# Optimization experiments

Hardware: AMD Instinct MI355X
Metric: run time of the kernel (lower is better)

## Reference

```python
import jax, jax.numpy as jnp
import numpy as np

B, H, W, C = 16, 64, 64, 256
WS = 8          # window_size
SHIFT = 4       # shift_size
HEADS = 8
HEAD_DIM = C // HEADS
N = WS * WS     # tokens per window
HID = 4 * C     # mlp hidden
EPS = 1e-5


def _rel_pos_index():
    coords = np.stack(np.meshgrid(np.arange(WS), np.arange(WS), indexing='ij'))  # [2,WS,WS]
    flat = coords.reshape(2, -1)                                                  # [2,N]
    rel = (flat[:, :, None] - flat[:, None, :]).transpose(1, 2, 0)                # [N,N,2]
    rel[:, :, 0] += WS - 1
    rel[:, :, 1] += WS - 1
    rel[:, :, 0] *= 2 * WS - 1
    return rel.sum(-1).astype(np.int32)                                           # [N,N]


def _attn_mask():
    # shifted-window region ids, identical to get_img_mask (shift == WS//2)
    img = np.zeros((H, W), dtype=np.float32)
    cnt = 0
    for hs in (slice(0, H - WS), slice(H - WS, H - SHIFT), slice(H - SHIFT, H)):
        for ws_ in (slice(0, W - WS), slice(W - WS, W - SHIFT), slice(W - SHIFT, W)):
            img[hs, ws_] = cnt
            cnt += 1
    mw = img.reshape(H // WS, WS, W // WS, WS).transpose(0, 2, 1, 3).reshape(-1, N)  # [nW,N]
    diff = mw[:, None, :] - mw[:, :, None]
    return np.where(diff != 0, -100.0, 0.0).astype(np.float32)                        # [nW,N,N]


def window_partition(x):
    # [B,H,W,C] -> [B*nW, N, C]
    x = x.reshape(B, H // WS, WS, W // WS, WS, C)
    return x.transpose(0, 1, 3, 2, 4, 5).reshape(-1, N, C)


def window_reverse(w):
    # [B*nW, WS, WS, C] -> [B,H,W,C]
    x = w.reshape(B, H // WS, W // WS, WS, WS, C)
    return x.transpose(0, 1, 3, 2, 4, 5).reshape(B, H, W, C)


def layernorm(x, g, b):
    mu = jnp.mean(x, -1, keepdims=True)
    var = jnp.mean(jnp.square(x - mu), -1, keepdims=True)
    return (x - mu) * jax.lax.rsqrt(var + EPS) * g + b


def setup_inputs() -> dict:
    key = jax.random.key(0)
    ks = jax.random.split(key, 12)
    s = 0.02
    return {
        'x': jax.random.normal(ks[0], (B, H, W, C), jnp.float32),
        'ln1_g': jnp.ones((C,), jnp.float32),
        'ln1_b': jnp.zeros((C,), jnp.float32),
        'qkv_w': jax.random.normal(ks[1], (C, 3 * C), jnp.float32) * s,
        'qkv_b': jnp.zeros((3 * C,), jnp.float32),
        'proj_w': jax.random.normal(ks[2], (C, C), jnp.float32) * s,
        'proj_b': jnp.zeros((C,), jnp.float32),
        'rel_bias_table': jax.random.normal(ks[3], ((2 * WS - 1) ** 2, HEADS), jnp.float32) * s,
        'ln2_g': jnp.ones((C,), jnp.float32),
        'ln2_b': jnp.zeros((C,), jnp.float32),
        'mlp_w1': jax.random.normal(ks[4], (C, HID), jnp.float32) * s,
        'mlp_b1': jnp.zeros((HID,), jnp.float32),
        'mlp_w2': jax.random.normal(ks[5], (HID, C), jnp.float32) * s,
        'mlp_b2': jnp.zeros((C,), jnp.float32),
        'rel_index': jnp.asarray(_rel_pos_index()),  # [N,N] int32, constant
    }


def reference(x, ln1_g, ln1_b, qkv_w, qkv_b, proj_w, proj_b, rel_bias_table,
              ln2_g, ln2_b, mlp_w1, mlp_b1, mlp_w2, mlp_b2, rel_index):
    attn_mask = jnp.asarray(_attn_mask())                 # [nW,N,N]
    nW = attn_mask.shape[0]

    shortcut = x.reshape(B, H * W, C)
    h = layernorm(shortcut, ln1_g, ln1_b).reshape(B, H, W, C)

    # cyclic shift + window partition
    h = jnp.roll(h, shift=(-SHIFT, -SHIFT), axis=(1, 2))
    xw = window_partition(h)                              # [B*nW, N, C]

    # window attention with relative position bias
    qkv = xw @ qkv_w + qkv_b                              # [B*nW, N, 3C]
    qkv = qkv.reshape(-1, N, 3, HEADS, HEAD_DIM).transpose(2, 0, 3, 1, 4)
    q, k, v = qkv[0], qkv[1], qkv[2]                      # [B*nW, heads, N, hd]
    attn = jnp.einsum('whnd,whmd->whnm', q * (HEAD_DIM ** -0.5), k)
    bias = rel_bias_table[rel_index]                      # [N,N,heads]
    attn = attn + bias.transpose(2, 0, 1)[None]           # [B*nW,heads,N,N]
    attn = attn.reshape(B, nW, HEADS, N, N) + attn_mask[None, :, None]
    attn = jax.nn.softmax(attn.reshape(-1, HEADS, N, N), axis=-1)
    out = jnp.einsum('whnm,whmd->whnd', attn, v)
    out = out.transpose(0, 2, 1, 3).reshape(-1, N, C)
    out = out @ proj_w + proj_b                           # [B*nW, N, C]

    # window reverse + reverse shift
    out = window_reverse(out.reshape(-1, WS, WS, C))
    out = jnp.roll(out, shift=(SHIFT, SHIFT), axis=(1, 2)).reshape(B, H * W, C)

    h = shortcut + out
    m = layernorm(h, ln2_g, ln2_b)
    m = jax.nn.gelu(m @ mlp_w1 + mlp_b1) @ mlp_w2 + mlp_b2
    h = h + m
    return h.reshape(B, H, W, C)
```

## Files before the change

kernel.cpp:

```cpp
#include <hip/hip_runtime.h>


typedef __attribute__((ext_vector_type(8))) short bf16x8;
typedef __attribute__((ext_vector_type(4))) float f32x4;
typedef __attribute__((ext_vector_type(16))) float f32x16;

__device__ __forceinline__ float bf2f(unsigned short h) {
    union { unsigned int u; float f; } c; c.u = ((unsigned int)h) << 16; return c.f;
}
__device__ __forceinline__ unsigned short f2bf(float f) {
    union { float f; unsigned int u; } c; c.f = f;
    unsigned int u = c.u;
    return (unsigned short)((u + 0x7FFFu + ((u >> 16) & 1u)) >> 16);
}
__device__ __forceinline__ unsigned int cvtpk_bf16(float lo, float hi) {
    unsigned int r;
    asm volatile("v_cvt_pk_bf16_f32 %0, %1, %2" : "=v"(r) : "v"(lo), "v"(hi));
    return r;
}
__device__ __forceinline__ void perm32swap(unsigned int& a, unsigned int& b) {
    asm volatile("v_permlane32_swap_b32 %0, %1" : "+v"(a), "+v"(b));
}
__device__ __forceinline__ int remap_row(int row) {
    int b  = row >> 12;
    int w6 = (row >> 6) & 63;
    int n  = row & 63;
    int hp = (((w6 >> 3) << 3) + (n >> 3) + 4) & 63;
    int wp = (((w6 & 7) << 3) + (n & 7) + 4) & 63;
    return (b << 12) | (hp << 6) | wp;
}
__device__ __forceinline__ float gelu_f(float v) {
    float u = 1.5957691216057308f * (v + 0.044715f * v * v * v);
    return v / (1.0f + __expf(-u));
}
__device__ __forceinline__ void gload16(const unsigned short* g, unsigned short* l) {
    __builtin_amdgcn_global_load_lds(
        (const __attribute__((address_space(1))) void*)g,
        (__attribute__((address_space(3))) void*)l, 16, 0, 0);
}

template<int INBF>
__global__ __launch_bounds__(256) void ln_kernel(
    const void* __restrict__ inp, const float* __restrict__ g,
    const float* __restrict__ b, unsigned short* __restrict__ out, int remap)
{
    int wave = threadIdx.x >> 6, lane = threadIdx.x & 63;
    int row = (blockIdx.x << 2) + wave;
    int src = remap ? remap_row(row) : row;
    float4 xv;
    if (INBF) {
        ushort4 u = *(const ushort4*)((const unsigned short*)inp + (size_t)src * 256 + (lane << 2));
        xv.x = bf2f(u.x); xv.y = bf2f(u.y); xv.z = bf2f(u.z); xv.w = bf2f(u.w);
    } else {
        xv = *(const float4*)((const float*)inp + (size_t)src * 256 + (lane << 2));
    }
    float s  = xv.x + xv.y + xv.z + xv.w;
    float ss = xv.x*xv.x + xv.y*xv.y + xv.z*xv.z + xv.w*xv.w;
#pragma unroll
    for (int off = 32; off; off >>= 1) {
        s  += __shfl_xor(s,  off, 64);
        ss += __shfl_xor(ss, off, 64);
    }
    float mu  = s * (1.0f / 256.0f);
    float inv = rsqrtf(ss * (1.0f / 256.0f) - mu * mu + 1e-5f);
    float4 gv = *(const float4*)(g + (lane << 2));
    float4 bv = *(const float4*)(b + (lane << 2));
    ushort4 o;
    o.x = f2bf((xv.x - mu) * inv * gv.x + bv.x);
    o.y = f2bf((xv.y - mu) * inv * gv.y + bv.y);
    o.z = f2bf((xv.z - mu) * inv * gv.z + bv.z);
    o.w = f2bf((xv.w - mu) * inv * gv.w + bv.w);
    *(ushort4*)(out + (size_t)row * 256 + (lane << 2)) = o;
}

__device__ __forceinline__ void convT_body(
    const float* __restrict__ in, unsigned short* __restrict__ out,
    int K, int N, int b, float (*t)[33], int tid)
{
    int kb = K >> 5;
    int bk = (b % kb) << 5;
    int bn = (b / kb) << 5;
    int r = tid >> 5, c = tid & 31;
#pragma unroll
    for (int i = 0; i < 4; ++i)
        t[r + i * 8][c] = in[(size_t)(bk + r + i * 8) * N + bn + c];
    __syncthreads();
#pragma unroll
    for (int i = 0; i < 4; ++i)
        out[(size_t)(bn + r + i * 8) * K + bk + c] = f2bf(t[c][r + i * 8]);
}

__global__ __launch_bounds__(256) void prep_kernel(
    const float* __restrict__ qkv_w, const float* __restrict__ proj_w,
    const float* __restrict__ w1, const float* __restrict__ w2,
    unsigned short* __restrict__ qkvT, unsigned short* __restrict__ prjT,
    unsigned short* __restrict__ w1T, unsigned short* __restrict__ w2T,
    const float* __restrict__ table, const int* __restrict__ relidx,
    float* __restrict__ bexp)
{
    __shared__ float t[32][33];
    const int b = blockIdx.x, tid = threadIdx.x;
    if      (b < 192) convT_body(qkv_w, qkvT, 256,  768, b,       t, tid);
    else if (b < 256) convT_body(proj_w, prjT, 256,  256, b - 192, t, tid);
    else if (b < 512) convT_body(w1,    w1T,  256, 1024, b - 256, t, tid);
    else if (b < 768) convT_body(w2,    w2T, 1024,  256, b - 512, t, tid);
    else {
        int i = (b - 768) * 256 + tid;
        int head = i >> 12;
        int q = (i >> 6) & 63;
        int k = i & 63;
        bexp[i] = table[relidx[q * 64 + k] * 8 + head];
    }
}

template<int OUT_BF16, int DO_GELU, int RESID, int QSCALE, int RESBF>
__global__ __launch_bounds__(512, 2) void mgemm_kernel(
    const unsigned short* __restrict__ A, const unsigned short* __restrict__ BT,
    const float* __restrict__ bias, void* __restrict__ outp,
    const void* __restrict__ resid, int M, int N, int K)
{
    __shared__ __align__(16) unsigned short smem[32768];
#define ASB(b) (smem + (b) * 4096)
#define BSB(b) (smem + 16384 + (b) * 4096)

    const int cpx = (int)gridDim.x >> 3;
    const int bid = ((int)blockIdx.x & 7) * cpx + ((int)blockIdx.x >> 3);

    const int nb = N >> 7;
    const int m0 = (bid / nb) << 7;
    const int n0 = (bid % nb) << 7;
    const int tid  = threadIdx.x;
    const int wid  = tid >> 6;
    const int lane = tid & 63;
    const int wm = (wid >> 1) << 5;
    const int wn = (wid & 1) << 6;

    const unsigned short* Ag = A  + (size_t)m0 * K;
    const unsigned short* Bg = BT + (size_t)n0 * K;
    const size_t ra = (size_t)(tid >> 2) * K + (((tid & 3) ^ ((tid >> 2) & 3)) << 3);

    f32x4 acc[4][2] = {};
    const int fr = lane & 15;
    const int fq = lane >> 4;
    const int axor = ((fq ^ (fr & 3)) << 3);

#define STAGE(buf, kk)                                                        \
    {                                                                         \
        gload16(Ag + ra + (kk), ASB(buf) + tid * 8);                          \
        gload16(Bg + ra + (kk), BSB(buf) + tid * 8);                          \
    }

    const int NIT = K >> 5;
    STAGE(0, 0);
    STAGE(1, 32);
    STAGE(2, 64);

    for (int t = 0; t < NIT; ++t) {
        if (t + 2 < NIT)      asm volatile("s_waitcnt vmcnt(4)" ::: "memory");
        else if (t + 1 < NIT) asm volatile("s_waitcnt vmcnt(2)" ::: "memory");
        else                  asm volatile("s_waitcnt vmcnt(0)" ::: "memory");
        __builtin_amdgcn_s_barrier();

        const int cur = t & 3;
        bf16x8 af[2], bfr[4];
#pragma unroll
        for (int i = 0; i < 2; ++i)
            af[i] = *(const bf16x8*)(ASB(cur) + (wm + i * 16 + fr) * 32 + axor);
#pragma unroll
        for (int j = 0; j < 4; ++j)
            bfr[j] = *(const bf16x8*)(BSB(cur) + (wn + j * 16 + fr) * 32 + axor);
#pragma unroll
        for (int j = 0; j < 4; ++j)
#pragma unroll
            for (int i = 0; i < 2; ++i)
                acc[j][i] = __builtin_amdgcn_mfma_f32_16x16x32_bf16(
                    bfr[j], af[i], acc[j][i], 0, 0, 0);

        if (t + 3 < NIT) STAGE((t + 3) & 3, (t + 3) << 5);
    }
#undef STAGE

    __builtin_amdgcn_s_barrier();

#pragma unroll
    for (int j = 0; j < 4; ++j) {
        const int fc = wn + j * 16 + (fq << 2);
        const int gcol = n0 + fc;
        const float4 b4 = *(const float4*)(bias + gcol);
#pragma unroll
        for (int i = 0; i < 2; ++i) {
            const int row = wm + i * 16 + fr;
            float v0 = acc[j][i][0] + b4.x;
            float v1 = acc[j][i][1] + b4.y;
            float v2 = acc[j][i][2] + b4.z;
            float v3 = acc[j][i][3] + b4.w;
            if (QSCALE && gcol < 256) {
                v0 *= 0.17677669529663687f; v1 *= 0.17677669529663687f;
                v2 *= 0.17677669529663687f; v3 *= 0.17677669529663687f;
            }
            if (DO_GELU) {
                v0 = gelu_f(v0); v1 = gelu_f(v1); v2 = gelu_f(v2); v3 = gelu_f(v3);
            }
            if (OUT_BF16) {
                uint2 pp;
                pp.x = cvtpk_bf16(v0, v1);
                pp.y = cvtpk_bf16(v2, v3);
                const int u = (row << 5) + ((fc >> 2) ^ (row & 6));
                *(uint2*)((char*)smem + (size_t)u * 8) = pp;
            } else {
                float4 o4; o4.x = v0; o4.y = v1; o4.z = v2; o4.w = v3;
                const int u = (row << 5) + ((fc >> 2) ^ (row & 7));
                *(float4*)((char*)smem + (size_t)u * 16) = o4;
            }
        }
    }
    __builtin_amdgcn_s_barrier();

    if (OUT_BF16) {
#pragma unroll
        for (int p = 0; p < 4; ++p) {
            const int row = (p << 5) + (tid >> 4);
            const int q = tid & 15;
            const int u = (row << 5) + ((q << 1) ^ (row & 6));
            uint4 a = *(const uint4*)((const char*)smem + (size_t)u * 8);
            const int grow = m0 + row;
            const int orow = (RESID == 2) ? remap_row(grow) : grow;
            const int gcol = n0 + (q << 3);
            if (RESID) {
                float rv[8];
                if (RESBF) {
                    ushort4 ra_ = *(const ushort4*)((const unsigned short*)resid
                                                    + (size_t)orow * N + gcol);
                    ushort4 rb_ = *(const ushort4*)((const unsigned short*)resid
                                                    + (size_t)orow * N + gcol + 4);
                    rv[0]=bf2f(ra_.x); rv[1]=bf2f(ra_.y); rv[2]=bf2f(ra_.z); rv[3]=bf2f(ra_.w);
                    rv[4]=bf2f(rb_.x); rv[5]=bf2f(rb_.y); rv[6]=bf2f(rb_.z); rv[7]=bf2f(rb_.w);
                } else {
                    float4 ra_ = *(const float4*)((const float*)resid + (size_t)orow * N + gcol);
                    float4 rb_ = *(const float4*)((const float*)resid + (size_t)orow * N + gcol + 4);
                    rv[0]=ra_.x; rv[1]=ra_.y; rv[2]=ra_.z; rv[3]=ra_.w;
                    rv[4]=rb_.x; rv[5]=rb_.y; rv[6]=rb_.z; rv[7]=rb_.w;
                }
                const unsigned short* s = (const unsigned short*)&a;
                uint4 o;
                o.x = cvtpk_bf16(bf2f(s[0]) + rv[0], bf2f(s[1]) + rv[1]);
                o.y = cvtpk_bf16(bf2f(s[2]) + rv[2], bf2f(s[3]) + rv[3]);
                o.z = cvtpk_bf16(bf2f(s[4]) + rv[4], bf2f(s[5]) + rv[5]);
                o.w = cvtpk_bf16(bf2f(s[6]) + rv[6], bf2f(s[7]) + rv[7]);
                a = o;
            }
            *(uint4*)((unsigned short*)outp + (size_t)orow * N + gcol) = a;
        }
    } else {
#pragma unroll
        for (int p = 0; p < 8; ++p) {
            const int row = (p << 4) + (tid >> 5);
            const int q = tid & 31;
            const int u = (row << 5) + (q ^ (row & 7));
            float4 v = *(const float4*)((const char*)smem + (size_t)u * 16);
            const int grow = m0 + row;
            const int orow = (RESID == 2) ? remap_row(grow) : grow;
            const int gcol = n0 + (q << 2);
            if (RESID) {
                if (RESBF) {
                    ushort4 r4 = *(const ushort4*)((const unsigned short*)resid
                                                   + (size_t)orow * N + gcol);
                    v.x += bf2f(r4.x); v.y += bf2f(r4.y);
                    v.z += bf2f(r4.z); v.w += bf2f(r4.w);
                } else {
                    float4 r4 = *(const float4*)((const float*)resid + (size_t)orow * N + gcol);
                    v.x += r4.x; v.y += r4.y; v.z += r4.z; v.w += r4.w;
                }
            }
            *(float4*)((float*)outp + (size_t)orow * N + gcol) = v;
        }
    }
#undef ASB
#undef BSB
}

__global__ __launch_bounds__(512, 1) void qkvattn_kernel(
    const unsigned short* __restrict__ xw,
    const unsigned short* __restrict__ qkvT,
    const float* __restrict__ qkv_b,
    const float* __restrict__ bexp,
    unsigned short* __restrict__ out)
{
    __shared__ __align__(16) unsigned short Asm[16384];
    const int widx = blockIdx.x;
    const int tid  = threadIdx.x;
    const int head = tid >> 6;
    const int l    = tid & 63;
    const int lo   = l & 31, hi = l >> 5;

    {
        const unsigned short* Ag = xw + ((size_t)widx << 6) * 256;
#pragma unroll
        for (int i = 0; i < 4; ++i) {
            int u = tid + (i << 9);
            int r = u >> 5, p = u & 31;
            int lg = (p & 24) | ((p ^ r) & 7);
            gload16(Ag + (size_t)r * 256 + lg * 8, Asm + u * 8);
        }
        asm volatile("s_waitcnt vmcnt(0)" ::: "memory");
        __builtin_amdgcn_s_barrier();
    }

#define AREAD(tok, kk)                                                         \
    (*(const bf16x8*)(Asm + (tok) * 256 +                                      \
        (((((kk) >> 3) + hi) & 24) | (((((kk) >> 3) + hi) ^ (tok)) & 7)) * 8))

#define DANCE(aa, op0, op1)                                                    \
    {                                                                          \
        _Pragma("unroll")                                                      \
        for (int kd_ = 0; kd_ < 2; ++kd_) {                                    \
            const int s8_ = kd_ * 8;                                           \
            unsigned int a0 = cvtpk_bf16((aa)[s8_ + 0], (aa)[s8_ + 1]);        \
            unsigned int b0 = cvtpk_bf16((aa)[s8_ + 4], (aa)[s8_ + 5]);        \
            unsigned int a1 = cvtpk_bf16((aa)[s8_ + 2], (aa)[s8_ + 3]);        \
            unsigned int b1 = cvtpk_bf16((aa)[s8_ + 6], (aa)[s8_ + 7]);        \
            perm32swap(a0, b0);                                                \
            perm32swap(a1, b1);                                                \
            union { unsigned int u[4]; bf16x8 v; } w_;                         \
            w_.u[0] = a0; w_.u[1] = a1; w_.u[2] = b0; w_.u[3] = b1;            \
            if (kd_) (op1) = w_.v; else (op0) = w_.v;                          \
        }                                                                      \
    }

    bf16x8 opK[2][2], opQ[2][2];

#pragma unroll
    for (int mat = 0; mat < 2; ++mat) {
        const int sec = mat ? 0 : 1;
        const unsigned short* Wb = qkvT + ((size_t)(sec * 256 + head * 32 + lo)) * 256 + 8 * hi;
        bf16x8 wf[16];
#pragma unroll
        for (int kk = 0; kk < 16; ++kk)
            wf[kk] = *(const bf16x8*)(Wb + kk * 16);
        f32x16 ac[2] = {};
#pragma unroll
        for (int kk = 0; kk < 16; ++kk) {
            ac[0] = __builtin_amdgcn_mfma_f32_32x32x16_bf16(
                wf[kk], AREAD(lo,      kk * 16), ac[0], 0, 0, 0);
            ac[1] = __builtin_amdgcn_mfma_f32_32x32x16_bf16(
                wf[kk], AREAD(lo + 32, kk * 16), ac[1], 0, 0, 0);
        }
        const float* bb = qkv_b + sec * 256 + head * 32 + 4 * hi;
#pragma unroll
        for (int tb = 0; tb < 2; ++tb) {
#pragma unroll
            for (int qd = 0; qd < 4; ++qd) {
                float4 b4 = *(const float4*)(bb + 8 * qd);
                ac[tb][4 * qd + 0] += b4.x;
                ac[tb][4 * qd + 1] += b4.y;
                ac[tb][4 * qd + 2] += b4.z;
                ac[tb][4 * qd + 3] += b4.w;
                if (sec == 0) {
                    ac[tb][4 * qd + 0] *= 0.17677669529663687f;
                    ac[tb][4 * qd + 1] *= 0.17677669529663687f;
                    ac[tb][4 * qd + 2] *= 0.17677669529663687f;
                    ac[tb][4 * qd + 3] *= 0.17677669529663687f;
                }
            }
            if (sec == 1) { DANCE(ac[tb], opK[tb][0], opK[tb][1]); }
            else          { DANCE(ac[tb], opQ[tb][0], opQ[tb][1]); }
        }
    }

    f32x16 acc[2][2] = {};
#pragma unroll
    for (int kd = 0; kd < 2; ++kd) {
        acc[0][0] = __builtin_amdgcn_mfma_f32_32x32x16_bf16(opK[0][kd], opQ[0][kd], acc[0][0], 0, 0, 0);
        acc[0][1] = __builtin_amdgcn_mfma_f32_32x32x16_bf16(opK[0][kd], opQ[1][kd], acc[0][1], 0, 0, 0);
        acc[1][0] = __builtin_amdgcn_mfma_f32_32x32x16_bf16(opK[1][kd], opQ[0][kd], acc[1][0], 0, 0, 0);
        acc[1][1] = __builtin_amdgcn_mfma_f32_32x32x16_bf16(opK[1][kd], opQ[1][kd], acc[1][1], 0, 0, 0);
    }

#pragma unroll
    for (int qb = 0; qb < 2; ++qb) {
        const float* bq = bexp + head * 4096 + (qb * 32 + lo) * 64;
#pragma unroll
        for (int kb = 0; kb < 2; ++kb)
#pragma unroll
            for (int j = 0; j < 4; ++j) {
                float4 b4 = *(const float4*)(bq + kb * 32 + j * 8 + hi * 4);
                acc[kb][qb][4 * j + 0] += b4.x;
                acc[kb][qb][4 * j + 1] += b4.y;
                acc[kb][qb][4 * j + 2] += b4.z;
                acc[kb][qb][4 * j + 3] += b4.w;
            }
    }

    const int w6 = widx & 63;
    if (((w6 >> 3) == 7) || ((w6 & 7) == 7)) {
#pragma unroll
        for (int qb = 0; qb < 2; ++qb) {
            int nq = qb * 32 + lo;
            int phq = ((w6 >> 3) << 3) + (nq >> 3), pwq = ((w6 & 7) << 3) + (nq & 7);
            int rq = ((phq < 56) ? 0 : ((phq < 60) ? 1 : 2)) * 3
                   + ((pwq < 56) ? 0 : ((pwq < 60) ? 1 : 2));
#pragma unroll
            for (int kb = 0; kb < 2; ++kb)
#pragma unroll
                for (int r = 0; r < 16; ++r) {
                    int nk = kb * 32 + (r & 3) + 8 * (r >> 2) + 4 * hi;
                    int phk = ((w6 >> 3) << 3) + (nk >> 3), pwk = ((w6 & 7) << 3) + (nk & 7);
                    int rk = ((phk < 56) ? 0 : ((phk < 60) ? 1 : 2)) * 3
                           + ((pwk < 56) ? 0 : ((pwk < 60) ? 1 : 2));
                    if (rk != rq) acc[kb][qb][r] -= 100.0f;
                }
        }
    }

#pragma unroll
    for (int qb = 0; qb < 2; ++qb) {
        float mx = acc[0][qb][0];
#pragma unroll
        for (int r = 1; r < 16; ++r) mx = fmaxf(mx, acc[0][qb][r]);
#pragma unroll
        for (int r = 0; r < 16; ++r) mx = fmaxf(mx, acc[1][qb][r]);
        mx = fmaxf(mx, __shfl_xor(mx, 32, 64));
        float sum = 0.f;
#pragma unroll
        for (int kb = 0; kb < 2; ++kb)
#pragma unroll
            for (int r = 0; r < 16; ++r) {
                float e = __expf(acc[kb][qb][r] - mx);
                acc[kb][qb][r] = e;
                sum += e;
            }
        sum += __shfl_xor(sum, 32, 64);
        float inv = 1.0f / sum;
#pragma unroll
        for (int kb = 0; kb < 2; ++kb)
#pragma unroll
            for (int r = 0; r < 16; ++r) acc[kb][qb][r] *= inv;
    }

    bf16x8 vop[2][2];
    {
        const unsigned short* Wb = qkvT + ((size_t)(512 + head * 32 + lo)) * 256 + 8 * hi;
        bf16x8 wf[16];
#pragma unroll
        for (int kk = 0; kk < 16; ++kk)
            wf[kk] = *(const bf16x8*)(Wb + kk * 16);
        f32x16 av[2] = {};
#pragma unroll
        for (int kk = 0; kk < 16; ++kk) {
            av[0] = __builtin_amdgcn_mfma_f32_32x32x16_bf16(
                AREAD(lo,      kk * 16), wf[kk], av[0], 0, 0, 0);
            av[1] = __builtin_amdgcn_mfma_f32_32x32x16_bf16(
                AREAD(lo + 32, kk * 16), wf[kk], av[1], 0, 0, 0);
        }
        const float bv = qkv_b[512 + head * 32 + lo];
#pragma unroll
        for (int tb = 0; tb < 2; ++tb) {
#pragma unroll
            for (int r = 0; r < 16; ++r) av[tb][r] += bv;
            DANCE(av[tb], vop[tb][0], vop[tb][1]);
        }
    }

    f32x16 o[2] = {};
#pragma unroll
    for (int ks = 0; ks < 4; ++ks) {
        const int s8 = (ks & 1) * 8, kb = ks >> 1;
        bf16x8 vb = vop[ks >> 1][ks & 1];
#pragma unroll
        for (int qb = 0; qb < 2; ++qb) {
            unsigned int a0 = cvtpk_bf16(acc[kb][qb][s8 + 0], acc[kb][qb][s8 + 1]);
            unsigned int b0 = cvtpk_bf16(acc[kb][qb][s8 + 4], acc[kb][qb][s8 + 5]);
            unsigned int a1 = cvtpk_bf16(acc[kb][qb][s8 + 2], acc[kb][qb][s8 + 3]);
            unsigned int b1 = cvtpk_bf16(acc[kb][qb][s8 + 6], acc[kb][qb][s8 + 7]);
            perm32swap(a0, b0);
            perm32swap(a1, b1);
            union { unsigned int u[4]; bf16x8 v; } w;
            w.u[0] = a0; w.u[1] = a1; w.u[2] = b0; w.u[3] = b1;
            o[qb] = __builtin_amdgcn_mfma_f32_32x32x16_bf16(w.v, vb, o[qb], 0, 0, 0);
        }
    }

    __builtin_amdgcn_s_barrier();
#pragma unroll
    for (int qb = 0; qb < 2; ++qb)
#pragma unroll
        for (int r = 0; r < 16; ++r) {
            int q = qb * 32 + (r & 3) + 8 * (r >> 2) + 4 * hi;
            *(unsigned short*)((char*)Asm + q * 512 + head * 64 + lo * 2) = f2bf(o[qb][r]);
        }
    __builtin_amdgcn_s_barrier();
    {
        unsigned short* ob = out + ((size_t)widx << 6) * 256;
#pragma unroll
        for (int i = 0; i < 4; ++i) {
            int u = tid + (i << 9);
            uint4 vv = *(const uint4*)((const char*)Asm + (size_t)u * 16);
            *(uint4*)(ob + (size_t)(u >> 5) * 256 + (u & 31) * 8) = vv;
        }
    }
#undef AREAD
#undef DANCE
}

extern "C" void kernel_launch(void* const* d_in, const int* in_sizes, int n_in,
                              void* d_out, int out_size, void* d_ws, size_t ws_size,
                              hipStream_t stream)
{
    const float* x      = (const float*)d_in[0];
    const float* ln1_g  = (const float*)d_in[1];
    const float* ln1_b  = (const float*)d_in[2];
    const float* qkv_w  = (const float*)d_in[3];
    const float* qkv_b  = (const float*)d_in[4];
    const float* proj_w = (const float*)d_in[5];
    const float* proj_b = (const float*)d_in[6];
    const float* table  = (const float*)d_in[7];
    const float* ln2_g  = (const float*)d_in[8];
    const float* ln2_b  = (const float*)d_in[9];
    const float* w1     = (const float*)d_in[10];
    const float* b1     = (const float*)d_in[11];
    const float* w2     = (const float*)d_in[12];
    const float* b2     = (const float*)d_in[13];
    const int*   relidx = (const int*)d_in[14];
    float* out = (float*)d_out;

    char* w = (char*)d_ws;
    unsigned short* xw   = (unsigned short*)w;
    unsigned short* qkvb = (unsigned short*)(w + (32u << 20));
    unsigned short* h2b  = (unsigned short*)(w + (160u << 20));
    float*          bexp = (float*)(w + (224u << 20));
    unsigned short* qkvT = (unsigned short*)(w + (224u << 20) + (128u << 10));
    unsigned short* prjT = qkvT + 768 * 256;
    unsigned short* w1T  = prjT + 256 * 256;
    unsigned short* w2T  = w1T + 1024 * 256;

    prep_kernel<<<896, 256, 0, stream>>>(qkv_w, proj_w, w1, w2,
                                         qkvT, prjT, w1T, w2T,
                                         table, relidx, bexp);
    ln_kernel<0><<<16384, 256, 0, stream>>>(x, ln1_g, ln1_b, xw, 1);
    qkvattn_kernel<<<1024, 512, 0, stream>>>(xw, qkvT, qkv_b, bexp, qkvb);
    mgemm_kernel<1, 0, 2, 0, 0><<<512 * 2, 512, 0, stream>>>(
        qkvb, prjT, proj_b, (void*)h2b, x, 65536, 256, 256);
    ln_kernel<1><<<16384, 256, 0, stream>>>(h2b, ln2_g, ln2_b, xw, 0);
    mgemm_kernel<1, 1, 0, 0, 0><<<512 * 8, 512, 0, stream>>>(
        xw, w1T, b1, (void*)qkvb, nullptr, 65536, 1024, 256);
    mgemm_kernel<0, 0, 1, 0, 1><<<512 * 2, 512, 0, stream>>>(
        qkvb, w2T, b2, (void*)out, h2b, 65536, 256, 1024);
}
```

Before: 286.6 us.

## Rewrite MLP/proj GEMM with 4-wave blocks, register-loaded B, direct epilogue

Replaces the 512-thread GEMM with a 256-thread variant in which each wave computes a 64x64 tile. Only A is staged in shared memory; B fragments are loaded straight from global memory into double-buffered registers. K becomes a compile-time constant so the loop fully unrolls. The epilogue writes results and adds the residual directly from registers, dropping the shared-memory transpose, so stores are narrower and less coalesced. The aim is to cut LDS traffic and barriers and raise per-wave MFMA density, at the cost of more register pressure and uncoalesced B loads.

```diff
diff --git a/kernel.cpp b/kernel.cpp
--- a/kernel.cpp
+++ b/kernel.cpp
@@ -113,170 +113,125 @@
     }
 }
 
-template<int OUT_BF16, int DO_GELU, int RESID, int QSCALE, int RESBF>
-__global__ __launch_bounds__(512, 2) void mgemm_kernel(
+template<int OUT_BF16, int DO_GELU, int RESID, int RESBF, int KDIM>
+__global__ __launch_bounds__(256, 3) void wgemm_kernel(
     const unsigned short* __restrict__ A, const unsigned short* __restrict__ BT,
     const float* __restrict__ bias, void* __restrict__ outp,
-    const void* __restrict__ resid, int M, int N, int K)
+    const void* __restrict__ resid, int M, int N)
 {
-    __shared__ __align__(16) unsigned short smem[32768];
-#define ASB(b) (smem + (b) * 4096)
-#define BSB(b) (smem + 16384 + (b) * 4096)
+    constexpr int NIT = KDIM >> 5;
+    __shared__ __align__(16) unsigned short As[4][128 * 32];
 
     const int cpx = (int)gridDim.x >> 3;
     const int bid = ((int)blockIdx.x & 7) * cpx + ((int)blockIdx.x >> 3);
-
     const int nb = N >> 7;
     const int m0 = (bid / nb) << 7;
     const int n0 = (bid % nb) << 7;
     const int tid  = threadIdx.x;
     const int wid  = tid >> 6;
     const int lane = tid & 63;
-    const int wm = (wid >> 1) << 5;
+    const int wm = (wid >> 1) << 6;
     const int wn = (wid & 1) << 6;
-
-    const unsigned short* Ag = A  + (size_t)m0 * K;
-    const unsigned short* Bg = BT + (size_t)n0 * K;
-    const size_t ra = (size_t)(tid >> 2) * K + (((tid & 3) ^ ((tid >> 2) & 3)) << 3);
-
-    f32x4 acc[4][2] = {};
-    const int fr = lane & 15;
-    const int fq = lane >> 4;
-    const int axor = ((fq ^ (fr & 3)) << 3);
+    const int fr = lane & 15, fq = lane >> 4;
+
+    const unsigned short* Ag = A + (size_t)m0 * KDIM;
+    const size_t ra0 = (size_t)(tid >> 2) * KDIM + (((tid & 3) ^ ((tid >> 3) & 3)) << 3);
+    const size_t ra1 = ra0 + (size_t)64 * KDIM;
+
+    const unsigned short* Bb = BT + (size_t)(n0 + wn + fr) * KDIM + fq * 8;
+
+    f32x4 acc[4][4] = {};
 
 #define STAGE(buf, kk)                                                        \
     {                                                                         \
-        gload16(Ag + ra + (kk), ASB(buf) + tid * 8);                          \
-        gload16(Bg + ra + (kk), BSB(buf) + tid * 8);                          \
-    }
-
-    const int NIT = K >> 5;
+        gload16(Ag + ra0 + (kk), As[buf] + tid * 8);                          \
+        gload16(Ag + ra1 + (kk), As[buf] + (tid + 256) * 8);                  \
+    }
+#define LOADB(dst, kk)                                                        \
+    {                                                                         \
+        _Pragma("unroll")                                                     \
+        for (int j_ = 0; j_ < 4; ++j_)                                        \
+            dst[j_] = *(const bf16x8*)(Bb + (size_t)j_ * 16 * KDIM + (kk));   \
+    }
+
+    bf16x8 bA[4], bB[4];
     STAGE(0, 0);
     STAGE(1, 32);
+    LOADB(bA, 0);
     STAGE(2, 64);
 
+#pragma unroll
     for (int t = 0; t < NIT; ++t) {
-        if (t + 2 < NIT)      asm volatile("s_waitcnt vmcnt(4)" ::: "memory");
-        else if (t + 1 < NIT) asm volatile("s_waitcnt vmcnt(2)" ::: "memory");
-        else                  asm volatile("s_waitcnt vmcnt(0)" ::: "memory");
+        if (t == 0)            asm volatile("s_waitcnt vmcnt(8)"  ::: "memory");
+        else if (t + 2 < NIT)  asm volatile("s_waitcnt vmcnt(12)" ::: "memory");
+        else if (t + 1 < NIT)  asm volatile("s_waitcnt vmcnt(10)" ::: "memory");
+        else                   asm volatile("s_waitcnt vmcnt(8)"  ::: "memory");
         __builtin_amdgcn_s_barrier();
-
-        const int cur = t & 3;
-        bf16x8 af[2], bfr[4];
-#pragma unroll
-        for (int i = 0; i < 2; ++i)
-            af[i] = *(const bf16x8*)(ASB(cur) + (wm + i * 16 + fr) * 32 + axor);
+        __builtin_amdgcn_sched_barrier(0);
+
+        if (t + 1 < NIT) {
+            if (t & 1) { LOADB(bA, (t + 1) * 32) }
+            else       { LOADB(bB, (t + 1) * 32) }
+        }
+
+        bf16x8 af[4];
+#pragma unroll
+        for (int i = 0; i < 4; ++i) {
+            const int row = wm + i * 16 + fr;
+            af[i] = *(const bf16x8*)(As[t & 3] + row * 32 +
+                                     ((fq ^ ((row >> 1) & 3)) << 3));
+        }
 #pragma unroll
         for (int j = 0; j < 4; ++j)
-            bfr[j] = *(const bf16x8*)(BSB(cur) + (wn + j * 16 + fr) * 32 + axor);
-#pragma unroll
-        for (int j = 0; j < 4; ++j)
-#pragma unroll
-            for (int i = 0; i < 2; ++i)
+#pragma unroll
+            for (int i = 0; i < 4; ++i)
                 acc[j][i] = __builtin_amdgcn_mfma_f32_16x16x32_bf16(
-                    bfr[j], af[i], acc[j][i], 0, 0, 0);
+                    (t & 1) ? bB[j] : bA[j], af[i], acc[j][i], 0, 0, 0);
 
         if (t + 3 < NIT) STAGE((t + 3) & 3, (t + 3) << 5);
     }
 #undef STAGE
-
-    __builtin_amdgcn_s_barrier();
+#undef LOADB
 
 #pragma unroll
     for (int j = 0; j < 4; ++j) {
-        const int fc = wn + j * 16 + (fq << 2);
-        const int gcol = n0 + fc;
-        const float4 b4 = *(const float4*)(bias + gcol);
-#pragma unroll
-        for (int i = 0; i < 2; ++i) {
-            const int row = wm + i * 16 + fr;
+        const int colbase = n0 + wn + j * 16 + (fq << 2);
+        const float4 b4 = *(const float4*)(bias + colbase);
+#pragma unroll
+        for (int i = 0; i < 4; ++i) {
+            const int row = m0 + wm + i * 16 + fr;
             float v0 = acc[j][i][0] + b4.x;
             float v1 = acc[j][i][1] + b4.y;
             float v2 = acc[j][i][2] + b4.z;
             float v3 = acc[j][i][3] + b4.w;
-            if (QSCALE && gcol < 256) {
-                v0 *= 0.17677669529663687f; v1 *= 0.17677669529663687f;
-                v2 *= 0.17677669529663687f; v3 *= 0.17677669529663687f;
-            }
             if (DO_GELU) {
                 v0 = gelu_f(v0); v1 = gelu_f(v1); v2 = gelu_f(v2); v3 = gelu_f(v3);
+            }
+            const int orow = (RESID == 2) ? remap_row(row) : row;
+            if (RESID) {
+                if (RESBF) {
+                    ushort4 r4 = *(const ushort4*)((const unsigned short*)resid
+                                                   + (size_t)orow * N + colbase);
+                    v0 += bf2f(r4.x); v1 += bf2f(r4.y);
+                    v2 += bf2f(r4.z); v3 += bf2f(r4.w);
+                } else {
+                    const float4 r4 = *(const float4*)((const float*)resid
+                                                       + (size_t)orow * N + colbase);
+                    v0 += r4.x; v1 += r4.y; v2 += r4.z; v3 += r4.w;
+                }
             }
             if (OUT_BF16) {
                 uint2 pp;
                 pp.x = cvtpk_bf16(v0, v1);
                 pp.y = cvtpk_bf16(v2, v3);
-                const int u = (row << 5) + ((fc >> 2) ^ (row & 6));
-                *(uint2*)((char*)smem + (size_t)u * 8) = pp;
+                *(uint2*)((unsigned short*)outp + (size_t)orow * N + colbase) = pp;
             } else {
-                float4 o4; o4.x = v0; o4.y = v1; o4.z = v2; o4.w = v3;
-                const int u = (row << 5) + ((fc >> 2) ^ (row & 7));
-                *(float4*)((char*)smem + (size_t)u * 16) = o4;
+                float4 o4;
+                o4.x = v0; o4.y = v1; o4.z = v2; o4.w = v3;
+                *(float4*)((float*)outp + (size_t)orow * N + colbase) = o4;
             }
         }
     }
-    __builtin_amdgcn_s_barrier();
-
-    if (OUT_BF16) {
-#pragma unroll
-        for (int p = 0; p < 4; ++p) {
-            const int row = (p << 5) + (tid >> 4);
-            const int q = tid & 15;
-            const int u = (row << 5) + ((q << 1) ^ (row & 6));
-            uint4 a = *(const uint4*)((const char*)smem + (size_t)u * 8);
-            const int grow = m0 + row;
-            const int orow = (RESID == 2) ? remap_row(grow) : grow;
-            const int gcol = n0 + (q << 3);
-            if (RESID) {
-                float rv[8];
-                if (RESBF) {
-                    ushort4 ra_ = *(const ushort4*)((const unsigned short*)resid
-                                                    + (size_t)orow * N + gcol);
-                    ushort4 rb_ = *(const ushort4*)((const unsigned short*)resid
-                                                    + (size_t)orow * N + gcol + 4);
-                    rv[0]=bf2f(ra_.x); rv[1]=bf2f(ra_.y); rv[2]=bf2f(ra_.z); rv[3]=bf2f(ra_.w);
-                    rv[4]=bf2f(rb_.x); rv[5]=bf2f(rb_.y); rv[6]=bf2f(rb_.z); rv[7]=bf2f(rb_.w);
-                } else {
-                    float4 ra_ = *(const float4*)((const float*)resid + (size_t)orow * N + gcol);
-                    float4 rb_ = *(const float4*)((const float*)resid + (size_t)orow * N + gcol + 4);
-                    rv[0]=ra_.x; rv[1]=ra_.y; rv[2]=ra_.z; rv[3]=ra_.w;
-                    rv[4]=rb_.x; rv[5]=rb_.y; rv[6]=rb_.z; rv[7]=rb_.w;
-                }
-                const unsigned short* s = (const unsigned short*)&a;
-                uint4 o;
-                o.x = cvtpk_bf16(bf2f(s[0]) + rv[0], bf2f(s[1]) + rv[1]);
-                o.y = cvtpk_bf16(bf2f(s[2]) + rv[2], bf2f(s[3]) + rv[3]);
-                o.z = cvtpk_bf16(bf2f(s[4]) + rv[4], bf2f(s[5]) + rv[5]);
-                o.w = cvtpk_bf16(bf2f(s[6]) + rv[6], bf2f(s[7]) + rv[7]);
-                a = o;
-            }
-            *(uint4*)((unsigned short*)outp + (size_t)orow * N + gcol) = a;
-        }
-    } else {
-#pragma unroll
-        for (int p = 0; p < 8; ++p) {
-            const int row = (p << 4) + (tid >> 5);
-            const int q = tid & 31;
-            const int u = (row << 5) + (q ^ (row & 7));
-            float4 v = *(const float4*)((const char*)smem + (size_t)u * 16);
-            const int grow = m0 + row;
-            const int orow = (RESID == 2) ? remap_row(grow) : grow;
-            const int gcol = n0 + (q << 2);
-            if (RESID) {
-                if (RESBF) {
-                    ushort4 r4 = *(const ushort4*)((const unsigned short*)resid
-                                                   + (size_t)orow * N + gcol);
-                    v.x += bf2f(r4.x); v.y += bf2f(r4.y);
-                    v.z += bf2f(r4.z); v.w += bf2f(r4.w);
-                } else {
-                    float4 r4 = *(const float4*)((const float*)resid + (size_t)orow * N + gcol);
-                    v.x += r4.x; v.y += r4.y; v.z += r4.z; v.w += r4.w;
-                }
-            }
-            *(float4*)((float*)outp + (size_t)orow * N + gcol) = v;
-        }
-    }
-#undef ASB
-#undef BSB
 }
 
 __global__ __launch_bounds__(512, 1) void qkvattn_kernel(
@@ -538,11 +493,11 @@
                                          table, relidx, bexp);
     ln_kernel<0><<<16384, 256, 0, stream>>>(x, ln1_g, ln1_b, xw, 1);
     qkvattn_kernel<<<1024, 512, 0, stream>>>(xw, qkvT, qkv_b, bexp, qkvb);
-    mgemm_kernel<1, 0, 2, 0, 0><<<512 * 2, 512, 0, stream>>>(
-        qkvb, prjT, proj_b, (void*)h2b, x, 65536, 256, 256);
+    wgemm_kernel<1, 0, 2, 0, 256><<<1024, 256, 0, stream>>>(
+        qkvb, prjT, proj_b, (void*)h2b, x, 65536, 256);
     ln_kernel<1><<<16384, 256, 0, stream>>>(h2b, ln2_g, ln2_b, xw, 0);
-    mgemm_kernel<1, 1, 0, 0, 0><<<512 * 8, 512, 0, stream>>>(
-        xw, w1T, b1, (void*)qkvb, nullptr, 65536, 1024, 256);
-    mgemm_kernel<0, 0, 1, 0, 1><<<512 * 2, 512, 0, stream>>>(
-        qkvb, w2T, b2, (void*)out, h2b, 65536, 256, 1024);
-}
+    wgemm_kernel<1, 1, 0, 0, 256><<<4096, 256, 0, stream>>>(
+        xw, w1T, b1, (void*)qkvb, nullptr, 65536, 1024);
+    wgemm_kernel<0, 0, 1, 1, 1024><<<1024, 256, 0, stream>>>(
+        qkvb, w2T, b2, (void*)out, h2b, 65536, 256);
+}
```

Result: slower. 343.1 us (+19.7%).
